# Optimization experiments

Hardware: AMD Instinct MI355X
Metric: run time of the kernel (lower is better)

## Reference

```python
import jax, jax.numpy as jnp
import numpy as np

EMBED = 192
HEADS = 6
WIN = (7, 7, 7)
B = 256
NW = 64  # number of distinct window masks; b // NW = true batch
N = WIN[0] * WIN[1] * WIN[2]  # 343 tokens per window


def _rel_pos_index(win):
    # Faithful port of the torch buffer construction.
    coords = np.stack(np.meshgrid(np.arange(win[0]), np.arange(win[1]), np.arange(win[2]), indexing='ij'))
    cf = coords.reshape(3, -1)                     # [3, N]
    rel = cf[:, :, None] - cf[:, None, :]          # [3, N, N]
    rel = rel.transpose(1, 2, 0).copy()            # [N, N, 3]
    rel[..., 0] += win[0] - 1
    rel[..., 1] += win[1] - 1
    rel[..., 2] += win[2] - 1
    rel[..., 0] *= (2 * win[1] - 1) * (2 * win[2] - 1)
    rel[..., 1] *= (2 * win[2] - 1)
    return rel.sum(-1).astype(np.int32)            # [N, N]


def setup_inputs() -> dict:
    key = jax.random.key(0)
    ks = jax.random.split(key, 8)
    table_size = (2 * WIN[0] - 1) * (2 * WIN[1] - 1) * (2 * WIN[2] - 1)  # 2197
    return {
        'x_in': jax.random.normal(ks[0], (B, N, EMBED), dtype=jnp.float32),
        'x_cross': jax.random.normal(ks[1], (B, N, EMBED), dtype=jnp.float32),
        'mask': jnp.zeros((NW, N, N), dtype=jnp.float32),
        'q_w': jax.random.normal(ks[2], (EMBED, EMBED), dtype=jnp.float32) * 0.02,
        'kv_w': jax.random.normal(ks[3], (2 * EMBED, EMBED), dtype=jnp.float32) * 0.02,
        'proj_w': jax.random.normal(ks[4], (EMBED, EMBED), dtype=jnp.float32) * 0.02,
        'proj_b': jnp.zeros((EMBED,), dtype=jnp.float32),
        'bias_table': jax.random.normal(ks[5], (table_size, HEADS), dtype=jnp.float32) * 0.02,
        'rel_idx': jnp.asarray(_rel_pos_index(WIN)),
    }


def reference(x_in, x_cross, mask, q_w, kv_w, proj_w, proj_b, bias_table, rel_idx):
    b, n, c = x_in.shape
    h = HEADS
    hd = c // h
    scale = hd ** -0.5
    # Projections (torch Linear: y = x @ W^T), no qkv bias
    q = (x_in @ q_w.T).reshape(b, n, h, hd).transpose(0, 2, 1, 3) * scale   # [b,h,n,hd]
    kv = (x_cross @ kv_w.T).reshape(b, n, 2, h, hd)
    k = kv[:, :, 0].transpose(0, 2, 1, 3)                                   # [b,h,n,hd]
    v = kv[:, :, 1].transpose(0, 2, 1, 3)                                   # [b,h,n,hd]
    attn = jnp.einsum('bhqd,bhkd->bhqk', q, k)                              # [b,h,n,n]
    # Gathered relative position bias
    bias = bias_table[rel_idx[:n, :n].reshape(-1)].reshape(n, n, h).transpose(2, 0, 1)
    attn = attn + bias[None]
    # Window mask add: [b//nw, nw, h, n, n] + [1, nw, 1, n, n]
    nw = mask.shape[0]
    attn = attn.reshape(b // nw, nw, h, n, n) + mask[None, :, None]
    attn = attn.reshape(b, h, n, n)
    attn = jax.nn.softmax(attn, axis=-1)
    x = jnp.einsum('bhqk,bhkd->bhqd', attn, v).transpose(0, 2, 1, 3).reshape(b, n, c)
    return x @ proj_w.T + proj_b
```

## Files before the change

kernel.cpp:

```cpp
#include <hip/hip_runtime.h>

#define NTOK 343
#define NPAD 352
#define CEMB 192
#define NH   6
#define HD   32
#define NB   256
#define NWIN 64

typedef __attribute__((ext_vector_type(8))) short short8;
typedef __attribute__((ext_vector_type(4))) float f32x4;
typedef __attribute__((ext_vector_type(4))) unsigned int uint4v;

__device__ __forceinline__ unsigned short f2bf(float f) {
    unsigned int u = __builtin_bit_cast(unsigned int, f);
    u += 0x7fffu + ((u >> 16) & 1u);
    return (unsigned short)(u >> 16);
}
__device__ __forceinline__ float bf2f(unsigned short h) {
    unsigned int u = ((unsigned int)h) << 16;
    return __builtin_bit_cast(float, u);
}
__device__ __forceinline__ short8 pack8(float4 f0, float4 f1) {
    short8 r;
    r[0] = (short)f2bf(f0.x); r[1] = (short)f2bf(f0.y);
    r[2] = (short)f2bf(f0.z); r[3] = (short)f2bf(f0.w);
    r[4] = (short)f2bf(f1.x); r[5] = (short)f2bf(f1.y);
    r[6] = (short)f2bf(f1.z); r[7] = (short)f2bf(f1.w);
    return r;
}
__device__ __forceinline__ unsigned int cvt_pk_bf16(float lo, float hi) {
    unsigned int r;
    asm("v_cvt_pk_bf16_f32 %0, %1, %2" : "=v"(r) : "v"(lo), "v"(hi));
    return r;
}

__global__ void prep_weights(const float* __restrict__ qw, const float* __restrict__ kvw,
                             const float* __restrict__ pw,
                             unsigned short* __restrict__ qwb, unsigned short* __restrict__ kvwb,
                             unsigned short* __restrict__ pwb) {
    const float scale = 0.17677669529663689f;
    int idx = blockIdx.x * 256 + threadIdx.x;
    if (idx < 36864)        qwb[idx] = f2bf(qw[idx] * scale);
    else if (idx < 110592)  kvwb[idx - 36864] = f2bf(kvw[idx - 36864]);
    else if (idx < 147456)  pwb[idx - 110592] = f2bf(pw[idx - 110592]);
}

__global__ void prep_biasN(const float* __restrict__ table, const int* __restrict__ rel,
                           unsigned short* __restrict__ biasN) {
    __shared__ int sidx[32 * 33];
    int bid = blockIdx.x;
    int qt = bid / 11, kt = bid - qt * 11;
    int q0 = qt * 32, k0 = kt * 32;
    for (int e = threadIdx.x; e < 1024; e += 256) {
        int i = e >> 5, j = e & 31;
        int q = q0 + i, k = k0 + j;
        sidx[i * 33 + j] = (q < NTOK && k < NTOK) ? rel[q * NTOK + k] : -1;
    }
    __syncthreads();
    for (int h = 0; h < NH; h++) {
        for (int e = threadIdx.x; e < 1024; e += 256) {
            int qq = e >> 5, kk = e & 31;
            int idx = sidx[qq * 33 + kk];
            float v = (idx >= 0) ? table[idx * NH + h] : 0.f;
            biasN[((size_t)h * NPAD + (q0 + qq)) * NPAD + (k0 + kk)] = f2bf(v);
        }
    }
}

__global__ void prep_maskN(const float* __restrict__ mask, unsigned short* __restrict__ maskN) {
    int idx = blockIdx.x * 256 + threadIdx.x;
    int w = idx / (NPAD * NPAD);
    int rem = idx - w * (NPAD * NPAD);
    int q = rem / NPAD, k = rem - q * NPAD;
    float v = (q < NTOK && k < NTOK) ? mask[((size_t)w * NTOK + q) * NTOK + k] : 0.f;
    maskN[idx] = f2bf(v);
}

__global__ __launch_bounds__(512, 2)
void qkv_kernel(const float* __restrict__ x_in, const float* __restrict__ x_cross,
                const unsigned short* __restrict__ qwb, const unsigned short* __restrict__ kvwb,
                unsigned short* __restrict__ Qb, unsigned short* __restrict__ Kb,
                unsigned short* __restrict__ Vtb) {
    extern __shared__ char smem[];
    unsigned short* Ws = (unsigned short*)smem;
    const int tid = threadIdx.x;
    const int wave = tid >> 6, lane = tid & 63;
    const int quad = lane >> 4, l16 = lane & 15;
    const int b = blockIdx.x / 3, o = blockIdx.x % 3;
    const float* xsrc = (o == 0) ? x_in : x_cross;
    const unsigned short* wsrc = (o == 0) ? qwb : (o == 1 ? kvwb : (kvwb + 192 * CEMB));
    const f32x4 zero4 = {0.f, 0.f, 0.f, 0.f};

    for (int i = tid; i < 4608; i += 512) {
        int r = i / 24, c8 = i - r * 24;
        *(short8*)(Ws + r * 200 + c8 * 8) = *(const short8*)(wsrc + (size_t)r * CEMB + c8 * 8);
    }
    __syncthreads();

    for (int mi = 0; mi < 3; mi++) {
        int mt = wave + (mi << 3);
        if (mt >= 22) continue;
        int row = mt * 16 + l16;
        f32x4 acc[12];
#pragma unroll
        for (int nt = 0; nt < 12; nt++) acc[nt] = zero4;
#pragma unroll
        for (int kc = 0; kc < 6; kc++) {
            short8 a = {};
            if (row < NTOK) {
                const float* xp = xsrc + ((size_t)b * NTOK + row) * CEMB + kc * 32 + (quad << 3);
                float4 f0 = *(const float4*)xp;
                float4 f1 = *(const float4*)(xp + 4);
                a = pack8(f0, f1);
            }
#pragma unroll
            for (int nt = 0; nt < 12; nt++) {
                const short8 bf = *(const short8*)(Ws + (nt * 16 + l16) * 200 + kc * 32 + (quad << 3));
                acc[nt] = __builtin_amdgcn_mfma_f32_16x16x32_bf16(a, bf, acc[nt], 0, 0, 0);
            }
        }
        if (o < 2) {
            unsigned short* dst = (o == 0 ? Qb : Kb) + (size_t)b * NPAD * CEMB;
#pragma unroll
            for (int nt = 0; nt < 12; nt++) {
#pragma unroll
                for (int r = 0; r < 4; r++) {
                    int m = mt * 16 + (quad << 2) + r;
                    dst[(size_t)m * CEMB + nt * 16 + l16] = f2bf(acc[nt][r]);
                }
            }
        } else {
#pragma unroll
            for (int nt = 0; nt < 12; nt++) {
                int h = nt >> 1, d = ((nt & 1) << 4) + l16;
#pragma unroll
                for (int r = 0; r < 4; r++) {
                    int m = mt * 16 + (quad << 2) + r;
                    Vtb[(((size_t)b * NH + h) * 32 + d) * 360 + m] = f2bf(acc[nt][r]);
                }
            }
        }
    }
}

__global__ __launch_bounds__(512, 6)
void attn_kernel(const unsigned short* __restrict__ Qb, const unsigned short* __restrict__ Kb,
                 const unsigned short* __restrict__ Vtb,
                 const unsigned short* __restrict__ biasN, const unsigned short* __restrict__ maskN,
                 unsigned short* __restrict__ attnb) {
    extern __shared__ char smem[];
    unsigned short* Ks = (unsigned short*)smem;
    unsigned short* Vt = (unsigned short*)(smem + 28160);

    const int tid = threadIdx.x;
    const int wave = tid >> 6, lane = tid & 63;
    const int quad = lane >> 4, l16 = lane & 15;
    const int q4 = quad << 2, q8 = quad << 3;
    const int q0b = (lane >> 4) & 1;
    const int q1b = (lane >> 5) & 1;
    const int b = blockIdx.x / NH, h = blockIdx.x - (blockIdx.x / NH) * NH;
    const f32x4 zero4 = {0.f, 0.f, 0.f, 0.f};

    for (int i = tid; i < 1408; i += 512) {
        int key = i >> 2, part = i & 3;
        *(short8*)(Ks + key * 40 + part * 8) =
            *(const short8*)(Kb + ((size_t)b * NPAD + key) * CEMB + h * 32 + part * 8);
    }
    const unsigned short* vsrc = Vtb + (size_t)(b * NH + h) * 32 * 360;
    for (int i = tid; i < 1440; i += 512) {
        *(short8*)(Vt + i * 8) = *(const short8*)(vsrc + i * 8);
    }
    short8 qa[3] = {};
#pragma unroll
    for (int i = 0; i < 3; i++) {
        int mt = wave + (i << 3);
        if (mt < 22)
            qa[i] = *(const short8*)(Qb + ((size_t)b * NPAD + mt * 16 + l16) * CEMB + h * 32 + q8);
    }
    __syncthreads();

    const unsigned short* biasNp = biasN + (size_t)h * NPAD * NPAD;
    const unsigned short* maskNp = maskN + (size_t)(b & 63) * NPAD * NPAD;
#pragma unroll
    for (int i = 0; i < 3; i++) {
        int mt = wave + (i << 3);
        if (mt >= 22) continue;
        const int q = mt * 16 + l16;
        const unsigned short* brow = biasNp + (size_t)q * NPAD;
        const unsigned short* mrow = maskNp + (size_t)q * NPAD;
        float rp = 0.f;
        f32x4 o0 = zero4, o1 = zero4;
        for (int ch = 0; ch < 11; ch++) {
            const int kb_ = ch * 32;
            const short8 k0f = *(const short8*)(Ks + (kb_ + l16) * 40 + q8);
            const short8 k1f = *(const short8*)(Ks + (kb_ + 16 + l16) * 40 + q8);
            f32x4 s0 = __builtin_amdgcn_mfma_f32_16x16x32_bf16(k0f, qa[i], zero4, 0, 0, 0);
            f32x4 s1 = __builtin_amdgcn_mfma_f32_16x16x32_bf16(k1f, qa[i], zero4, 0, 0, 0);
            const ushort4 bt0 = *(const ushort4*)(brow + kb_ + q4);
            const ushort4 mk0 = *(const ushort4*)(mrow + kb_ + q4);
            const ushort4 bt1 = *(const ushort4*)(brow + kb_ + 16 + q4);
            const ushort4 mk1 = *(const ushort4*)(mrow + kb_ + 16 + q4);
            float p00 = __expf(s0[0] + bf2f(bt0.x) + bf2f(mk0.x));
            float p01 = __expf(s0[1] + bf2f(bt0.y) + bf2f(mk0.y));
            float p02 = __expf(s0[2] + bf2f(bt0.z) + bf2f(mk0.z));
            float p03 = __expf(s0[3] + bf2f(bt0.w) + bf2f(mk0.w));
            float p10 = __expf(s1[0] + bf2f(bt1.x) + bf2f(mk1.x));
            float p11 = __expf(s1[1] + bf2f(bt1.y) + bf2f(mk1.y));
            float p12 = __expf(s1[2] + bf2f(bt1.z) + bf2f(mk1.z));
            float p13 = __expf(s1[3] + bf2f(bt1.w) + bf2f(mk1.w));
            if (ch == 10) {
                if (q4 + 0 >= 7) p10 = 0.f;
                if (q4 + 1 >= 7) p11 = 0.f;
                if (q4 + 2 >= 7) p12 = 0.f;
                if (q4 + 3 >= 7) p13 = 0.f;
            }
            rp += ((p00 + p01) + (p02 + p03)) + ((p10 + p11) + (p12 + p13));
            unsigned int c0 = cvt_pk_bf16(p00, p01);
            unsigned int c1 = cvt_pk_bf16(p02, p03);
            unsigned int c2 = cvt_pk_bf16(p10, p11);
            unsigned int c3 = cvt_pk_bf16(p12, p13);
            unsigned int pe0 = q1b ? c0 : c2;
            unsigned int pe1 = q1b ? c1 : c3;
            unsigned int sh0 = __shfl_xor(pe0, 32);
            unsigned int sh1 = __shfl_xor(pe1, 32);
            unsigned int t0 = q1b ? sh0 : c0;
            unsigned int t1 = q1b ? sh1 : c1;
            unsigned int t2 = q1b ? c2 : sh0;
            unsigned int t3 = q1b ? c3 : sh1;
            unsigned int pf0 = q0b ? t0 : t2;
            unsigned int pf1 = q0b ? t1 : t3;
            unsigned int u0 = __shfl_xor(pf0, 16);
            unsigned int u1 = __shfl_xor(pf1, 16);
            unsigned int r0 = q0b ? u0 : t0;
            unsigned int r1 = q0b ? u1 : t1;
            unsigned int r2 = q0b ? t2 : u0;
            unsigned int r3 = q0b ? t3 : u1;
            const short8 pa = __builtin_bit_cast(short8, (uint4v){r0, r1, r2, r3});
            const short8 v0 = *(const short8*)(Vt + l16 * 360 + kb_ + q8);
            const short8 v1 = *(const short8*)(Vt + (16 + l16) * 360 + kb_ + q8);
            o0 = __builtin_amdgcn_mfma_f32_16x16x32_bf16(pa, v0, o0, 0, 0, 0);
            o1 = __builtin_amdgcn_mfma_f32_16x16x32_bf16(pa, v1, o1, 0, 0, 0);
        }
        rp += __shfl_xor(rp, 16);
        rp += __shfl_xor(rp, 32);
        float inv = 1.f / rp;
#pragma unroll
        for (int r = 0; r < 4; r++) {
            float invr = __shfl(inv, (lane & 48) | (q4 + r));
            int n = mt * 16 + q4 + r;
            if (n < NTOK) {
                size_t base = ((size_t)b * NTOK + n) * CEMB + h * 32;
                attnb[base + l16] = f2bf(o0[r] * invr);
                attnb[base + 16 + l16] = f2bf(o1[r] * invr);
            }
        }
    }
}

__global__ __launch_bounds__(512, 2)
void proj_kernel(const unsigned short* __restrict__ attnb, const unsigned short* __restrict__ pwb,
                 const float* __restrict__ proj_b, float* __restrict__ out) {
    extern __shared__ char smem[];
    unsigned short* Ws = (unsigned short*)smem;
    const int tid = threadIdx.x;
    const int wave = tid >> 6, lane = tid & 63;
    const int quad = lane >> 4, l16 = lane & 15;
    for (int i = tid; i < 4608; i += 512) {
        int r = i / 24, c8 = i - r * 24;
        *(short8*)(Ws + r * 200 + c8 * 8) = *(const short8*)(pwb + (size_t)r * CEMB + c8 * 8);
    }
    float pb[12];
#pragma unroll
    for (int nt = 0; nt < 12; nt++) pb[nt] = proj_b[nt * 16 + l16];
    __syncthreads();

    const int mt = blockIdx.x * 8 + wave;
    const f32x4 zero4 = {0.f, 0.f, 0.f, 0.f};
    f32x4 acc[12];
#pragma unroll
    for (int nt = 0; nt < 12; nt++) acc[nt] = zero4;
#pragma unroll
    for (int ks = 0; ks < 6; ks++) {
        const short8 a = *(const short8*)(attnb + ((size_t)mt * 16 + l16) * CEMB + ks * 32 + (quad << 3));
#pragma unroll
        for (int nt = 0; nt < 12; nt++) {
            const short8 bfrag = *(const short8*)(Ws + (nt * 16 + l16) * 200 + ks * 32 + (quad << 3));
            acc[nt] = __builtin_amdgcn_mfma_f32_16x16x32_bf16(a, bfrag, acc[nt], 0, 0, 0);
        }
    }
#pragma unroll
    for (int nt = 0; nt < 12; nt++) {
#pragma unroll
        for (int r = 0; r < 4; r++) {
            int m = mt * 16 + (quad << 2) + r;
            out[(size_t)m * CEMB + nt * 16 + l16] = acc[nt][r] + pb[nt];
        }
    }
}

extern "C" void kernel_launch(void* const* d_in, const int* in_sizes, int n_in,
                              void* d_out, int out_size, void* d_ws, size_t ws_size,
                              hipStream_t stream) {
    (void)in_sizes; (void)n_in; (void)out_size; (void)ws_size;
    const float* x_in    = (const float*)d_in[0];
    const float* x_cross = (const float*)d_in[1];
    const float* mask    = (const float*)d_in[2];
    const float* q_w     = (const float*)d_in[3];
    const float* kv_w    = (const float*)d_in[4];
    const float* proj_w  = (const float*)d_in[5];
    const float* proj_b  = (const float*)d_in[6];
    const float* btab    = (const float*)d_in[7];
    const int*   rel     = (const int*)d_in[8];
    float* out = (float*)d_out;
    char* ws = (char*)d_ws;

    unsigned short* qwb   = (unsigned short*)(ws + 0);
    unsigned short* kvwb  = (unsigned short*)(ws + 73728);
    unsigned short* pwb   = (unsigned short*)(ws + 221184);
    unsigned short* biasN = (unsigned short*)(ws + 294912);
    unsigned short* maskN = (unsigned short*)(ws + 1781760);
    unsigned short* attnb = (unsigned short*)(ws + 17641472);
    unsigned short* Qb    = (unsigned short*)(ws + 51359744);
    unsigned short* Kb    = (unsigned short*)(ws + 85962752);
    unsigned short* Vtb   = (unsigned short*)(ws + 120565760);

    prep_weights<<<576, 256, 0, stream>>>(q_w, kv_w, proj_w, qwb, kvwb, pwb);
    prep_biasN<<<121, 256, 0, stream>>>(btab, rel, biasN);
    prep_maskN<<<30976, 256, 0, stream>>>(mask, maskN);
    qkv_kernel<<<NB * 3, 512, 76800, stream>>>(x_in, x_cross, qwb, kvwb, Qb, Kb, Vtb);
    attn_kernel<<<NB * NH, 512, 51200, stream>>>(Qb, Kb, Vtb, biasN, maskN, attnb);
    proj_kernel<<<686, 512, 76800, stream>>>(attnb, pwb, proj_b, out);
}
```

Baseline: 419.8 us.

## Use exp2 with prescaled log2e, prefetch bias/mask, permlane swaps, remap block order

Folds log2(e) into the Q weight scale, bias table and mask so the softmax can use the native exp2 instruction instead of __expf. Prefetches the next chunk's bias and mask rows one iteration ahead to hide global load latency. Replaces the shuffle/select transpose of P with permlane32/permlane16 swap intrinsics. Remaps block indices so blocks sharing the same window mask run together, which should improve L2 reuse of the mask; the permlane fragment ordering must match the previous layout exactly.

```diff
diff --git a/kernel.cpp b/kernel.cpp
--- a/kernel.cpp
+++ b/kernel.cpp
@@ -11,6 +11,7 @@
 typedef __attribute__((ext_vector_type(8))) short short8;
 typedef __attribute__((ext_vector_type(4))) float f32x4;
 typedef __attribute__((ext_vector_type(4))) unsigned int uint4v;
+typedef __attribute__((ext_vector_type(2))) unsigned int uint2v;
 
 __device__ __forceinline__ unsigned short f2bf(float f) {
     unsigned int u = __builtin_bit_cast(unsigned int, f);
@@ -35,11 +36,13 @@
     return r;
 }
 
+#define LOG2E 1.4426950408889634f
+
 __global__ void prep_weights(const float* __restrict__ qw, const float* __restrict__ kvw,
                              const float* __restrict__ pw,
                              unsigned short* __restrict__ qwb, unsigned short* __restrict__ kvwb,
                              unsigned short* __restrict__ pwb) {
-    const float scale = 0.17677669529663689f;
+    const float scale = 0.17677669529663689f * LOG2E;
     int idx = blockIdx.x * 256 + threadIdx.x;
     if (idx < 36864)        qwb[idx] = f2bf(qw[idx] * scale);
     else if (idx < 110592)  kvwb[idx - 36864] = f2bf(kvw[idx - 36864]);
@@ -62,7 +65,7 @@
         for (int e = threadIdx.x; e < 1024; e += 256) {
             int qq = e >> 5, kk = e & 31;
             int idx = sidx[qq * 33 + kk];
-            float v = (idx >= 0) ? table[idx * NH + h] : 0.f;
+            float v = (idx >= 0) ? table[idx * NH + h] * LOG2E : 0.f;
             biasN[((size_t)h * NPAD + (q0 + qq)) * NPAD + (k0 + kk)] = f2bf(v);
         }
     }
@@ -73,7 +76,7 @@
     int w = idx / (NPAD * NPAD);
     int rem = idx - w * (NPAD * NPAD);
     int q = rem / NPAD, k = rem - q * NPAD;
-    float v = (q < NTOK && k < NTOK) ? mask[((size_t)w * NTOK + q) * NTOK + k] : 0.f;
+    float v = (q < NTOK && k < NTOK) ? mask[((size_t)w * NTOK + q) * NTOK + k] * LOG2E : 0.f;
     maskN[idx] = f2bf(v);
 }
 
@@ -157,9 +160,11 @@
     const int wave = tid >> 6, lane = tid & 63;
     const int quad = lane >> 4, l16 = lane & 15;
     const int q4 = quad << 2, q8 = quad << 3;
-    const int q0b = (lane >> 4) & 1;
-    const int q1b = (lane >> 5) & 1;
-    const int b = blockIdx.x / NH, h = blockIdx.x - (blockIdx.x / NH) * NH;
+    const int p = blockIdx.x;
+    const int L = (p & 7) * 192 + (p >> 3);
+    const int w = L / 24, r_ = L - w * 24;
+    const int b = (r_ / 6) * 64 + w;
+    const int h = r_ - (r_ / 6) * 6;
     const f32x4 zero4 = {0.f, 0.f, 0.f, 0.f};
 
     for (int i = tid; i < 1408; i += 512) {
@@ -181,7 +186,7 @@
     __syncthreads();
 
     const unsigned short* biasNp = biasN + (size_t)h * NPAD * NPAD;
-    const unsigned short* maskNp = maskN + (size_t)(b & 63) * NPAD * NPAD;
+    const unsigned short* maskNp = maskN + (size_t)w * NPAD * NPAD;
 #pragma unroll
     for (int i = 0; i < 3; i++) {
         int mt = wave + (i << 3);
@@ -191,24 +196,29 @@
         const unsigned short* mrow = maskNp + (size_t)q * NPAD;
         float rp = 0.f;
         f32x4 o0 = zero4, o1 = zero4;
+        ushort4 bt0c = *(const ushort4*)(brow + q4);
+        ushort4 mk0c = *(const ushort4*)(mrow + q4);
+        ushort4 bt1c = *(const ushort4*)(brow + 16 + q4);
+        ushort4 mk1c = *(const ushort4*)(mrow + 16 + q4);
         for (int ch = 0; ch < 11; ch++) {
             const int kb_ = ch * 32;
+            const int kbn = (ch < 10) ? kb_ + 32 : kb_;
+            ushort4 bt0n = *(const ushort4*)(brow + kbn + q4);
+            ushort4 mk0n = *(const ushort4*)(mrow + kbn + q4);
+            ushort4 bt1n = *(const ushort4*)(brow + kbn + 16 + q4);
+            ushort4 mk1n = *(const ushort4*)(mrow + kbn + 16 + q4);
             const short8 k0f = *(const short8*)(Ks + (kb_ + l16) * 40 + q8);
             const short8 k1f = *(const short8*)(Ks + (kb_ + 16 + l16) * 40 + q8);
             f32x4 s0 = __builtin_amdgcn_mfma_f32_16x16x32_bf16(k0f, qa[i], zero4, 0, 0, 0);
             f32x4 s1 = __builtin_amdgcn_mfma_f32_16x16x32_bf16(k1f, qa[i], zero4, 0, 0, 0);
-            const ushort4 bt0 = *(const ushort4*)(brow + kb_ + q4);
-            const ushort4 mk0 = *(const ushort4*)(mrow + kb_ + q4);
-            const ushort4 bt1 = *(const ushort4*)(brow + kb_ + 16 + q4);
-            const ushort4 mk1 = *(const ushort4*)(mrow + kb_ + 16 + q4);
-            float p00 = __expf(s0[0] + bf2f(bt0.x) + bf2f(mk0.x));
-            float p01 = __expf(s0[1] + bf2f(bt0.y) + bf2f(mk0.y));
-            float p02 = __expf(s0[2] + bf2f(bt0.z) + bf2f(mk0.z));
-            float p03 = __expf(s0[3] + bf2f(bt0.w) + bf2f(mk0.w));
-            float p10 = __expf(s1[0] + bf2f(bt1.x) + bf2f(mk1.x));
-            float p11 = __expf(s1[1] + bf2f(bt1.y) + bf2f(mk1.y));
-            float p12 = __expf(s1[2] + bf2f(bt1.z) + bf2f(mk1.z));
-            float p13 = __expf(s1[3] + bf2f(bt1.w) + bf2f(mk1.w));
+            float p00 = __builtin_amdgcn_exp2f(s0[0] + bf2f(bt0c.x) + bf2f(mk0c.x));
+            float p01 = __builtin_amdgcn_exp2f(s0[1] + bf2f(bt0c.y) + bf2f(mk0c.y));
+            float p02 = __builtin_amdgcn_exp2f(s0[2] + bf2f(bt0c.z) + bf2f(mk0c.z));
+            float p03 = __builtin_amdgcn_exp2f(s0[3] + bf2f(bt0c.w) + bf2f(mk0c.w));
+            float p10 = __builtin_amdgcn_exp2f(s1[0] + bf2f(bt1c.x) + bf2f(mk1c.x));
+            float p11 = __builtin_amdgcn_exp2f(s1[1] + bf2f(bt1c.y) + bf2f(mk1c.y));
+            float p12 = __builtin_amdgcn_exp2f(s1[2] + bf2f(bt1c.z) + bf2f(mk1c.z));
+            float p13 = __builtin_amdgcn_exp2f(s1[3] + bf2f(bt1c.w) + bf2f(mk1c.w));
             if (ch == 10) {
                 if (q4 + 0 >= 7) p10 = 0.f;
                 if (q4 + 1 >= 7) p11 = 0.f;
@@ -220,27 +230,16 @@
             unsigned int c1 = cvt_pk_bf16(p02, p03);
             unsigned int c2 = cvt_pk_bf16(p10, p11);
             unsigned int c3 = cvt_pk_bf16(p12, p13);
-            unsigned int pe0 = q1b ? c0 : c2;
-            unsigned int pe1 = q1b ? c1 : c3;
-            unsigned int sh0 = __shfl_xor(pe0, 32);
-            unsigned int sh1 = __shfl_xor(pe1, 32);
-            unsigned int t0 = q1b ? sh0 : c0;
-            unsigned int t1 = q1b ? sh1 : c1;
-            unsigned int t2 = q1b ? c2 : sh0;
-            unsigned int t3 = q1b ? c3 : sh1;
-            unsigned int pf0 = q0b ? t0 : t2;
-            unsigned int pf1 = q0b ? t1 : t3;
-            unsigned int u0 = __shfl_xor(pf0, 16);
-            unsigned int u1 = __shfl_xor(pf1, 16);
-            unsigned int r0 = q0b ? u0 : t0;
-            unsigned int r1 = q0b ? u1 : t1;
-            unsigned int r2 = q0b ? t2 : u0;
-            unsigned int r3 = q0b ? t3 : u1;
-            const short8 pa = __builtin_bit_cast(short8, (uint4v){r0, r1, r2, r3});
+            uint2v sa = __builtin_amdgcn_permlane32_swap(c0, c2, false, false);
+            uint2v sb = __builtin_amdgcn_permlane32_swap(c1, c3, false, false);
+            uint2v ta = __builtin_amdgcn_permlane16_swap(sa[0], sa[1], false, false);
+            uint2v tb = __builtin_amdgcn_permlane16_swap(sb[0], sb[1], false, false);
+            const short8 pa = __builtin_bit_cast(short8, (uint4v){ta[0], tb[0], ta[1], tb[1]});
             const short8 v0 = *(const short8*)(Vt + l16 * 360 + kb_ + q8);
             const short8 v1 = *(const short8*)(Vt + (16 + l16) * 360 + kb_ + q8);
             o0 = __builtin_amdgcn_mfma_f32_16x16x32_bf16(pa, v0, o0, 0, 0, 0);
             o1 = __builtin_amdgcn_mfma_f32_16x16x32_bf16(pa, v1, o1, 0, 0, 0);
+            bt0c = bt0n; mk0c = mk0n; bt1c = bt1n; mk1c = mk1n;
         }
         rp += __shfl_xor(rp, 16);
         rp += __shfl_xor(rp, 32);
```

Measured after the change: 411.5 us. 2.0% less time.
